# Kernel optimization log

Measured on AMD Instinct MI355X. Metric: run time of the kernel, lower is better.

The kernel has to match this reference:

```python
import jax, jax.numpy as jnp
import numpy as np

EMB = 64
HID = 1024
SEQ = 9
BATCH = 4096


def setup_inputs() -> dict:
    key = jax.random.key(0)
    ks = jax.random.split(key, 10)
    s = lambda *sh: 1.0 / np.sqrt(sh[-1])
    return {
        "observed": jax.random.normal(ks[0], (SEQ, BATCH, 2), dtype=jnp.float32),
        "W_emb": jax.random.normal(ks[1], (EMB, 2), dtype=jnp.float32) * s(2),
        "b_emb": jnp.zeros((EMB,), dtype=jnp.float32),
        "W_ih": jax.random.normal(ks[2], (4 * HID, EMB), dtype=jnp.float32) * s(EMB),
        "b_ih": jnp.zeros((4 * HID,), dtype=jnp.float32),
        "W_hh": jax.random.normal(ks[3], (4 * HID, HID), dtype=jnp.float32) * s(HID),
        "b_hh": jnp.zeros((4 * HID,), dtype=jnp.float32),
        "W_out": jax.random.normal(ks[4], (5, HID), dtype=jnp.float32) * s(HID),
        "b_out": jnp.zeros((5,), dtype=jnp.float32),
        "n_predict": 12,
    }


def _cell(x, h, c, W_ih, b_ih, W_hh, b_hh):
    # torch.nn.LSTMCell gate math, gate order i, f, g, o
    gates = x @ W_ih.T + b_ih + h @ W_hh.T + b_hh  # [B, 4H]
    i, f, g, o = jnp.split(gates, 4, axis=-1)
    c_new = jax.nn.sigmoid(f) * c + jax.nn.sigmoid(i) * jnp.tanh(g)
    h_new = jax.nn.sigmoid(o) * jnp.tanh(c_new)
    return h_new, c_new


def reference(observed, W_emb, b_emb, W_ih, b_ih, W_hh, b_hh, W_out, b_out, n_predict):
    B = observed.shape[1]
    H = W_hh.shape[1]
    h0 = jnp.zeros((B, H), dtype=observed.dtype)
    c0 = jnp.zeros((B, H), dtype=observed.dtype)

    diffs = observed[1:] - observed[:-1]  # [SEQ-1, B, 2]

    def obs_step(carry, d):
        h, c = carry
        emb = jax.nn.relu(d @ W_emb.T + b_emb)  # [B, EMB]
        h, c = _cell(emb, h, c, W_ih, b_ih, W_hh, b_hh)
        normal = h @ W_out.T + b_out  # [B, 5]
        return (h, c), normal

    (h, c), normals_obs = jax.lax.scan(obs_step, (h0, c0), diffs)
    new_vel = normals_obs[-1][:, :2]

    def pred_step(carry, _):
        h, c, nv = carry
        emb = jax.nn.relu(jax.lax.stop_gradient(nv) @ W_emb.T + b_emb)
        h, c = _cell(emb, h, c, W_ih, b_ih, W_hh, b_hh)
        normal = h @ W_out.T + b_out
        return (h, c, normal[:, :2]), normal

    (_, _, _), normals_pred = jax.lax.scan(
        pred_step, (h, c, new_vel), None, length=n_predict - 1)

    # training-mode output: stacked raw 'normal' params, shape [SEQ-1+n_predict-1, B, 5]
    return jnp.concatenate([normals_obs, normals_pred], axis=0)
```

## Files before the change

### kernel.cpp

```cpp
#include <hip/hip_runtime.h>
#include <stdint.h>
#include <stddef.h>

#define BATCH 4096
#define HID   1024
#define EMB   64
#define NKH   32
#define NSTEP 19
#define NOBS  8
#define WSL   139264

typedef _Float16 f16;
typedef _Float16 half8 __attribute__((ext_vector_type(8)));
typedef float    float4v __attribute__((ext_vector_type(4)));

__device__ __forceinline__ float sigm(float x) { return 1.f / (1.f + __expf(-x)); }
__device__ __forceinline__ float tanh_f(float x) { return 1.f - 2.f / (__expf(2.f * x) + 1.f); }

typedef const __attribute__((address_space(1))) unsigned int gau32;
typedef __attribute__((address_space(3))) unsigned int lau32;

__device__ __forceinline__ void gload16(const void* src, void* lds) {
  __builtin_amdgcn_global_load_lds((gau32*)src, (lau32*)lds, 16, 0, 0);
}

__global__ void pack_kernel(const float* __restrict__ W_ih, const float* __restrict__ b_ih,
                            const float* __restrict__ W_hh, const float* __restrict__ b_hh,
                            f16* __restrict__ Wsw, float* __restrict__ bc) {
  int gid = blockIdx.x * blockDim.x + threadIdx.x;
  int tt = gid / WSL;
  int rem = gid - tt * WSL;
  int kt = rem >> 12;
  int ni = (rem >> 9) & 7;
  int lane = (rem >> 3) & 63;
  int e = rem & 7;
  int p = tt * 128 + ni * 16 + (lane & 15);
  int g = (p >> 4) & 3;
  int u = (p >> 8) * 64 + ((p >> 6) & 3) * 16 + (p & 15);
  int orig = g * HID + u;
  int k = kt * 32 + ((lane >> 4) << 3) + e;
  float val = (k < EMB) ? W_ih[orig * EMB + k] : W_hh[orig * HID + (k - EMB)];
  Wsw[gid] = (f16)val;
  if (k == 0) bc[p] = b_ih[orig] + b_hh[orig];
}

__global__ __launch_bounds__(512, 2)
void gemm_cell_kernel(const f16* __restrict__ Xp, const f16* __restrict__ Wsw,
                      const float* __restrict__ bc,
                      f16* __restrict__ c_ws, f16* __restrict__ Xn,
                      float* __restrict__ po_ws, const float* __restrict__ W_out,
                      const float* __restrict__ obs_t, const float* __restrict__ outprev,
                      int mode, const float* __restrict__ W_emb,
                      const float* __restrict__ b_emb) {
  __shared__ f16 smem[65536];

  const int tid = threadIdx.x;
  const int lane = tid & 63;
  const int w = tid >> 6;
  const int l15 = lane & 15;
  const int quad = lane >> 4;
  const int wm = w >> 2, wn = w & 3;
  const int sh = wn >> 1, nq = wn & 1;

  const int id = blockIdx.x;
  const int x = id & 7, rr0 = id >> 3;
  const int bn = x * 2 + (rr0 & 1);
  const int bm = rr0 >> 1;
  const int slice = bn * 2 + sh;

  float4v acc[8][4];
#pragma unroll
  for (int mi = 0; mi < 8; ++mi)
#pragma unroll
    for (int ni = 0; ni < 4; ++ni) acc[mi][ni] = (float4v){0.f, 0.f, 0.f, 0.f};

  auto stage = [&](int sp) {
    const int p2 = sp & 1;
    const int khg = 2 * (sp - 1);
#pragma unroll
    for (int i = 0; i < 4; ++i) {
      const int c = wn * 4 + i;
      const int rtl = wm * 8 + (c >> 1), khl = c & 1;
      const f16* src = Xp + ((size_t)(bm * 16 + rtl) * NKH + (khg + khl)) * 512 + lane * 8;
      f16* dst = smem + p2 * 32768 + (rtl * 2 + khl) * 512;
      gload16(src, dst);
    }
#pragma unroll
    for (int i = 0; i < 4; ++i) {
      const int c = (wm * 2 + nq) * 4 + i;
      const int nisl = c >> 1, khl = c & 1;
      const f16* src = Wsw + (size_t)slice * WSL + (2 + khg + khl) * 4096 + nisl * 512 + lane * 8;
      f16* dst = smem + p2 * 32768 + 16384 + ((sh * 8 + nisl) * 2 + khl) * 512;
      gload16(src, dst);
    }
  };

  if (mode != 0) stage(1);

  {
    float d0[8], d1[8];
#pragma unroll
    for (int mi = 0; mi < 8; ++mi) {
      const int row = (bm * 16 + wm * 8 + mi) * 16 + l15;
      if (mode <= 1) {
        const float* o = obs_t + (size_t)row * 2;
        d0[mi] = o[BATCH * 2] - o[0];
        d1[mi] = o[BATCH * 2 + 1] - o[1];
      } else {
        d0[mi] = outprev[(size_t)row * 5 + 0];
        d1[mi] = outprev[(size_t)row * 5 + 1];
      }
    }
#pragma unroll
    for (int kt = 0; kt < 2; ++kt) {
      float w0[8], w1[8], be[8];
#pragma unroll
      for (int e = 0; e < 8; ++e) {
        const int j = kt * 32 + quad * 8 + e;
        w0[e] = W_emb[2 * j];
        w1[e] = W_emb[2 * j + 1];
        be[e] = b_emb[j];
      }
      half8 bfe[4];
#pragma unroll
      for (int ni = 0; ni < 4; ++ni)
        bfe[ni] = *(const half8*)(Wsw + (size_t)slice * WSL + kt * 4096 + (nq * 4 + ni) * 512 + lane * 8);
#pragma unroll
      for (int mi = 0; mi < 8; ++mi) {
        half8 ae;
#pragma unroll
        for (int e = 0; e < 8; ++e)
          ae[e] = (f16)fmaxf(d0[mi] * w0[e] + d1[mi] * w1[e] + be[e], 0.f);
#pragma unroll
        for (int ni = 0; ni < 4; ++ni)
          acc[mi][ni] = __builtin_amdgcn_mfma_f32_16x16x32_f16(ae, bfe[ni], acc[mi][ni], 0, 0, 0);
      }
    }
  }

  if (mode != 0) {
    for (int s = 1; s <= 16; ++s) {
      __syncthreads();
      if (s < 16) stage(s + 1);

      const f16* base = smem + (s & 1) * 32768;
#pragma unroll
      for (int khl = 0; khl < 2; ++khl) {
        half8 a[8], bq[4];
#pragma unroll
        for (int mi = 0; mi < 8; ++mi)
          a[mi] = *(const half8*)(base + ((wm * 8 + mi) * 2 + khl) * 512 + lane * 8);
#pragma unroll
        for (int ni = 0; ni < 4; ++ni)
          bq[ni] = *(const half8*)(base + 16384 + ((sh * 8 + nq * 4 + ni) * 2 + khl) * 512 + lane * 8);
        __builtin_amdgcn_s_setprio(1);
#pragma unroll
        for (int mi = 0; mi < 8; ++mi)
#pragma unroll
          for (int ni = 0; ni < 4; ++ni)
            acc[mi][ni] =
                __builtin_amdgcn_mfma_f32_16x16x32_f16(a[mi], bq[ni], acc[mi][ni], 0, 0, 0);
        __builtin_amdgcn_s_setprio(0);
      }
    }
  }

  float bb[4];
#pragma unroll
  for (int ni = 0; ni < 4; ++ni) bb[ni] = bc[bn * 256 + wn * 64 + ni * 16 + l15];
  const int u = bn * 64 + wn * 16 + l15;
  float wo[5];
#pragma unroll
  for (int o = 0; o < 5; ++o) wo[o] = W_out[o * HID + u];

  f16* cbase = c_ws + (((size_t)(bm * 16 + bn) * 8 + w) * 64 + lane) * 32;
  half8 cv[4];
  if (mode != 0) {
#pragma unroll
    for (int q = 0; q < 4; ++q) cv[q] = *(const half8*)(cbase + q * 8);
  }

  __syncthreads();
  float* pol = (float*)smem;

#pragma unroll
  for (int mi = 0; mi < 8; ++mi) {
#pragma unroll
    for (int r = 0; r < 4; ++r) {
      const int rl = wm * 128 + mi * 16 + quad * 4 + r;
      const int row = bm * 256 + rl;
      const int ci = mi * 4 + r;
      float gi = acc[mi][0][r] + bb[0];
      float gf = acc[mi][1][r] + bb[1];
      float gg = acc[mi][2][r] + bb[2];
      float go = acc[mi][3][r] + bb[3];
      float co = (mode == 0) ? 0.f : (float)cv[ci >> 3][ci & 7];
      float cn = sigm(gf) * co + sigm(gi) * tanh_f(gg);
      cv[ci >> 3][ci & 7] = (f16)cn;
      float h = sigm(go) * tanh_f(cn);
      Xn[(((size_t)(row >> 4) * NKH + slice) * 64 + (quad * 4 + r) +
          16 * ((wn & 1) * 2 + (l15 >> 3))) * 8 + (l15 & 7)] = (f16)h;
      float pa[5];
#pragma unroll
      for (int o = 0; o < 5; ++o) pa[o] = h * wo[o];
#pragma unroll
      for (int o = 0; o < 5; ++o) {
        pa[o] += __shfl_xor(pa[o], 1, 64);
        pa[o] += __shfl_xor(pa[o], 2, 64);
        pa[o] += __shfl_xor(pa[o], 4, 64);
        pa[o] += __shfl_xor(pa[o], 8, 64);
      }
      if (l15 == 0) {
#pragma unroll
        for (int o = 0; o < 5; ++o) pol[(rl * 4 + wn) * 5 + o] = pa[o];
      }
    }
  }
#pragma unroll
  for (int q = 0; q < 4; ++q) *(half8*)(cbase + q * 8) = cv[q];

  __syncthreads();
  for (int idx = tid; idx < 1280; idx += 512) {
    const int rl = idx / 5, o = idx - rl * 5;
    float s = 0.f;
#pragma unroll
    for (int j = 0; j < 4; ++j) s += pol[(rl * 4 + j) * 5 + o];
    po_ws[((size_t)bn * BATCH + bm * 256 + rl) * 5 + o] = s;
  }
}

__global__ __launch_bounds__(256)
void reduce_kernel(const float* __restrict__ po_ws, const float* __restrict__ b_out,
                   float* __restrict__ out_t) {
  const int tid = threadIdx.x;
  const int r0 = blockIdx.x * 32;
  if (tid < 160) {
    const int rowl = tid / 5, o = tid - rowl * 5;
    const int row = r0 + rowl;
    float s = 0.f;
#pragma unroll
    for (int g = 0; g < 16; ++g) s += po_ws[((size_t)g * BATCH + row) * 5 + o];
    out_t[(size_t)row * 5 + o] = s + b_out[o];
  }
}

extern "C" void kernel_launch(void* const* d_in, const int* in_sizes, int n_in,
                              void* d_out, int out_size, void* d_ws, size_t ws_size,
                              hipStream_t stream) {
  const float* observed = (const float*)d_in[0];
  const float* W_emb = (const float*)d_in[1];
  const float* b_emb = (const float*)d_in[2];
  const float* W_ih = (const float*)d_in[3];
  const float* b_ih = (const float*)d_in[4];
  const float* W_hh = (const float*)d_in[5];
  const float* b_hh = (const float*)d_in[6];
  const float* W_out = (const float*)d_in[7];
  const float* b_out = (const float*)d_in[8];
  float* out = (float*)d_out;

  uint8_t* ws = (uint8_t*)d_ws;
  const size_t WSW_BYTES = (size_t)32 * WSL * sizeof(f16);
  const size_t XH_BYTES = (size_t)256 * NKH * 64 * 8 * sizeof(f16);
  f16* Wsw = (f16*)ws;
  float* bc = (float*)(ws + WSW_BYTES);
  f16* X0 = (f16*)(ws + WSW_BYTES + 16384);
  f16* X1 = (f16*)(ws + WSW_BYTES + 16384 + XH_BYTES);
  f16* c_ws = (f16*)(ws + WSW_BYTES + 16384 + 2 * XH_BYTES);
  float* po_ws = (float*)(ws + WSW_BYTES + 16384 + 2 * XH_BYTES + (size_t)BATCH * HID * 2);

  pack_kernel<<<(32 * WSL) / 256, 256, 0, stream>>>(W_ih, b_ih, W_hh, b_hh, Wsw, bc);

  for (int t = 0; t < NSTEP; ++t) {
    f16* Xc = (t & 1) ? X1 : X0;
    f16* Xq = (t & 1) ? X0 : X1;
    const int mode = (t == 0) ? 0 : (t < NOBS ? 1 : 2);
    gemm_cell_kernel<<<256, 512, 0, stream>>>(
        Xq, Wsw, bc, c_ws, Xc, po_ws, W_out,
        observed + (size_t)t * BATCH * 2, out + (size_t)(t - 1) * BATCH * 5,
        mode, W_emb, b_emb);
    reduce_kernel<<<BATCH / 32, 256, 0, stream>>>(po_ws, b_out, out + (size_t)t * BATCH * 5);
  }
}
```

Before: 1.134 ms.

## Deepen recurrent GEMM pipeline to four LDS stages with explicit vmcnt waits

Restructures the hidden-state GEMM K loop from a double-buffered loop over pairs of K chunks into a four-buffer ring with one K chunk per stage. Loads are issued three stages ahead, and the code waits on them with explicit s_waitcnt vmcnt counts and raw barriers instead of __syncthreads. The goal is to hide global-to-LDS latency behind MFMA work and to cut full barrier drains. In exchange it runs twice as many barrier iterations, and correctness depends on the hand-set vmcnt counts matching the number of outstanding loads per stage.

```diff
diff --git a/kernel.cpp b/kernel.cpp
--- a/kernel.cpp
+++ b/kernel.cpp
@@ -75,27 +75,37 @@
     for (int ni = 0; ni < 4; ++ni) acc[mi][ni] = (float4v){0.f, 0.f, 0.f, 0.f};
 
   auto stage = [&](int sp) {
-    const int p2 = sp & 1;
-    const int khg = 2 * (sp - 1);
-#pragma unroll
-    for (int i = 0; i < 4; ++i) {
-      const int c = wn * 4 + i;
-      const int rtl = wm * 8 + (c >> 1), khl = c & 1;
-      const f16* src = Xp + ((size_t)(bm * 16 + rtl) * NKH + (khg + khl)) * 512 + lane * 8;
-      f16* dst = smem + p2 * 32768 + (rtl * 2 + khl) * 512;
-      gload16(src, dst);
-    }
-#pragma unroll
-    for (int i = 0; i < 4; ++i) {
-      const int c = (wm * 2 + nq) * 4 + i;
-      const int nisl = c >> 1, khl = c & 1;
-      const f16* src = Wsw + (size_t)slice * WSL + (2 + khg + khl) * 4096 + nisl * 512 + lane * 8;
-      f16* dst = smem + p2 * 32768 + 16384 + ((sh * 8 + nisl) * 2 + khl) * 512;
-      gload16(src, dst);
+    const int bix = ((sp - 1) & 3) * 16384;
+    const int kh = sp - 1;
+#pragma unroll
+    for (int i = 0; i < 2; ++i) {
+      const int rtl = w * 2 + i;
+      gload16(Xp + ((size_t)(bm * 16 + rtl) * NKH + kh) * 512 + lane * 8,
+              smem + bix + rtl * 512);
+      const int shn = w * 2 + i;
+      gload16(Wsw + (size_t)(bn * 2 + (shn >> 3)) * WSL + (2 + kh) * 4096 + (shn & 7) * 512 +
+                  lane * 8,
+              smem + bix + 8192 + shn * 512);
     }
   };
 
-  if (mode != 0) stage(1);
+  auto compute = [&](int s) {
+    const f16* base = smem + ((s - 1) & 3) * 16384;
+    half8 a[8], bq[4];
+#pragma unroll
+    for (int mi = 0; mi < 8; ++mi)
+      a[mi] = *(const half8*)(base + (wm * 8 + mi) * 512 + lane * 8);
+#pragma unroll
+    for (int ni = 0; ni < 4; ++ni)
+      bq[ni] = *(const half8*)(base + 8192 + (sh * 8 + nq * 4 + ni) * 512 + lane * 8);
+    __builtin_amdgcn_s_setprio(1);
+#pragma unroll
+    for (int mi = 0; mi < 8; ++mi)
+#pragma unroll
+      for (int ni = 0; ni < 4; ++ni)
+        acc[mi][ni] = __builtin_amdgcn_mfma_f32_16x16x32_f16(a[mi], bq[ni], acc[mi][ni], 0, 0, 0);
+    __builtin_amdgcn_s_setprio(0);
+  };
 
   {
     float d0[8], d1[8];
@@ -139,30 +149,29 @@
   }
 
   if (mode != 0) {
-    for (int s = 1; s <= 16; ++s) {
-      __syncthreads();
-      if (s < 16) stage(s + 1);
-
-      const f16* base = smem + (s & 1) * 32768;
-#pragma unroll
-      for (int khl = 0; khl < 2; ++khl) {
-        half8 a[8], bq[4];
-#pragma unroll
-        for (int mi = 0; mi < 8; ++mi)
-          a[mi] = *(const half8*)(base + ((wm * 8 + mi) * 2 + khl) * 512 + lane * 8);
-#pragma unroll
-        for (int ni = 0; ni < 4; ++ni)
-          bq[ni] = *(const half8*)(base + 16384 + ((sh * 8 + nq * 4 + ni) * 2 + khl) * 512 + lane * 8);
-        __builtin_amdgcn_s_setprio(1);
-#pragma unroll
-        for (int mi = 0; mi < 8; ++mi)
-#pragma unroll
-          for (int ni = 0; ni < 4; ++ni)
-            acc[mi][ni] =
-                __builtin_amdgcn_mfma_f32_16x16x32_f16(a[mi], bq[ni], acc[mi][ni], 0, 0, 0);
-        __builtin_amdgcn_s_setprio(0);
-      }
-    }
+    asm volatile("s_waitcnt vmcnt(0)" ::: "memory");
+    stage(1);
+    stage(2);
+    stage(3);
+    for (int s = 1; s <= 29; ++s) {
+      asm volatile("s_waitcnt vmcnt(8)" ::: "memory");
+      __builtin_amdgcn_s_barrier();
+      __builtin_amdgcn_sched_barrier(0);
+      stage(s + 3);
+      compute(s);
+    }
+    asm volatile("s_waitcnt vmcnt(8)" ::: "memory");
+    __builtin_amdgcn_s_barrier();
+    __builtin_amdgcn_sched_barrier(0);
+    compute(30);
+    asm volatile("s_waitcnt vmcnt(4)" ::: "memory");
+    __builtin_amdgcn_s_barrier();
+    __builtin_amdgcn_sched_barrier(0);
+    compute(31);
+    asm volatile("s_waitcnt vmcnt(0)" ::: "memory");
+    __builtin_amdgcn_s_barrier();
+    __builtin_amdgcn_sched_barrier(0);
+    compute(32);
   }
 
   float bb[4];
```

Measured after the change: 1.136 ms. Within noise of the previous version (+0.1%).
